# Performance work log

Hardware: AMD Instinct MI355X
Metric: run time of the kernel (lower is better)

The kernel has to match this reference:

```python
import jax, jax.numpy as jnp
import numpy as np

B, S, D, E, K = 4, 4096, 2048, 64, 2


def setup_inputs() -> dict:
    key = jax.random.key(0)
    kx, kwg, kwn, kn = jax.random.split(key, 4)
    scale = 1.0 / np.sqrt(D)
    return {
        "x": jax.random.normal(kx, (B, S, D), dtype=jnp.float32),
        "Wg": jax.random.normal(kwg, (E, D), dtype=jnp.float32) * scale,
        "bg": jnp.zeros((E,), dtype=jnp.float32),
        "Wn": jax.random.normal(kwn, (E, D), dtype=jnp.float32) * scale,
        "bn": jnp.zeros((E,), dtype=jnp.float32),
        "noise": jax.random.normal(kn, (B, S, E), dtype=jnp.float32),
    }


def reference(x, Wg, bg, Wn, bn, noise):
    # gate / noise projections: [B,S,D] @ [D,E] -> [B,S,E]
    gate_logits = jnp.einsum("bsd,ed->bse", x, Wg) + bg
    noise_std = jax.nn.softplus(jnp.einsum("bsd,ed->bse", x, Wn) + bn)
    noisy_logits = gate_logits + noise * noise_std  # training-mode path

    # top-k over experts, then scatter back with -inf elsewhere
    flat = noisy_logits.reshape(-1, E)  # [T, E], T = B*S
    top_vals, top_idx = jax.lax.top_k(flat, K)  # [T, K]
    T = flat.shape[0]
    neg_inf = jnp.full((T, E), -jnp.inf, dtype=flat.dtype)
    full_logits = neg_inf.at[jnp.arange(T)[:, None], top_idx].set(top_vals)

    gate_probs = jax.nn.softmax(full_logits, axis=-1).reshape(B, S, E)
    top_k_indices = top_idx.reshape(B, S, K)
    return gate_probs, top_k_indices
```

## Files before the change

### kernel.cpp

```cpp
#include <hip/hip_runtime.h>
#include <math.h>
#include <stdint.h>

#define D_ 2048
#define E_ 64
#define T_ 16384

#define BM 64
#define BK 64
#define NT 32
#define ABUF_B 16384
#define BBUF_B 32768
#define BUF_B (ABUF_B + BBUF_B)
#define CT_STRIDE 132

typedef _Float16 h8 __attribute__((ext_vector_type(8)));
typedef float f16v __attribute__((ext_vector_type(16)));

__device__ __forceinline__ void split2(const float4& a, const float4& b,
                                       h8& h, h8& m) {
    const float xe[8] = {a.x, a.y, a.z, a.w, b.x, b.y, b.z, b.w};
#pragma unroll
    for (int i = 0; i < 8; ++i) {
        const _Float16 hh_ = (_Float16)xe[i];
        const float r = (xe[i] - (float)hh_) * 1024.0f;
        h[i] = hh_;
        m[i] = (_Float16)r;
    }
}

__device__ __forceinline__ void gload16(const void* g, void* l) {
    __builtin_amdgcn_global_load_lds(
        (const __attribute__((address_space(1))) uint32_t*)g,
        (__attribute__((address_space(3))) uint32_t*)l, 16, 0, 0);
}

__device__ __forceinline__ void topk_epilogue(float g, float nl, float nz,
                                              int lane, size_t tg,
                                              float* __restrict__ out_probs,
                                              float* __restrict__ out_idx) {
    const float sp = fmaxf(nl, 0.f) + log1pf(expf(-fabsf(nl)));
    const float noisy = g + nz * sp;

    float v = noisy;
    int idx = lane;
#pragma unroll
    for (int off = 32; off > 0; off >>= 1) {
        const float ov = __shfl_xor(v, off);
        const int oi = __shfl_xor(idx, off);
        if (ov > v || (ov == v && oi < idx)) { v = ov; idx = oi; }
    }
    const float v1 = v;
    const int i1 = idx;
    v = (lane == i1) ? -INFINITY : noisy;
    idx = lane;
#pragma unroll
    for (int off = 32; off > 0; off >>= 1) {
        const float ov = __shfl_xor(v, off);
        const int oi = __shfl_xor(idx, off);
        if (ov > v || (ov == v && oi < idx)) { v = ov; idx = oi; }
    }
    const float v2 = v;
    const int i2 = idx;

    const float e2 = expf(v2 - v1);
    const float denom = 1.f + e2;
    const float p = (lane == i1) ? (1.f / denom)
                                 : ((lane == i2) ? (e2 / denom) : 0.f);
    out_probs[tg * E_ + lane] = p;
    if (lane == 0) {
        out_idx[tg * 2 + 0] = (float)i1;
        out_idx[tg * 2 + 1] = (float)i2;
    }
}

__global__ void w_split_kernel(const float* __restrict__ Wg,
                               const float* __restrict__ Wn,
                               h8* __restrict__ wsp) {
    const int idx = blockIdx.x * blockDim.x + threadIdx.x;
    const int lane = idx & 63;
    const int s = (idx >> 6) & 127;
    const int f = idx >> 13;
    const int n = f * 32 + (lane & 31);
    const int k0 = s * 16 + ((lane >> 5) << 3);
    const float* src = (n < 64) ? &Wg[(size_t)n * D_ + k0]
                                : &Wn[(size_t)(n - 64) * D_ + k0];
    h8 hv, mv;
#pragma unroll
    for (int i = 0; i < 8; ++i) {
        const float w = src[i];
        const _Float16 wh = (_Float16)w;
        const float r = (w - (float)wh) * 1024.0f;
        hv[i] = wh;
        mv[i] = (_Float16)r;
    }
    wsp[0 * 32768 + idx] = hv;
    wsp[1 * 32768 + idx] = mv;
}

__launch_bounds__(512)
__global__ void gemm_topk_kernel(const float* __restrict__ x,
                                 const h8* __restrict__ wsp,
                                 const float* __restrict__ bg,
                                 const float* __restrict__ bn,
                                 const float* __restrict__ noise,
                                 float* __restrict__ out_probs,
                                 float* __restrict__ out_idx) {
    __shared__ __align__(16) char smem[2 * BUF_B];
    const int tid = threadIdx.x;
    const int lane = tid & 63;
    const int wv = tid >> 6;
    const int mh = wv >> 2;
    const int wn = wv & 3;
    const int block_m0 = blockIdx.x * BM;
    const char* wb = (const char*)wsp;

    const int smf = tid >> 8;
    const int sks = (tid >> 6) & 3;
    const int sl = tid & 63;
    const int srow = smf * 32 + (sl & 31);
    const float* asrc = x + (size_t)(block_m0 + srow) * D_
                          + sks * 16 + ((sl >> 5) << 3);
    const int aw_hi = (0 * 8 + smf * 4 + sks) * 1024 + sl * 16;
    const int aw_mid = (1 * 8 + smf * 4 + sks) * 1024 + sl * 16;

    f16v hh = {}, cx = {};

    auto STAGE_B = [&](int t, int b) {
        char* Bb = smem + b * BUF_B + ABUF_B;
#pragma unroll
        for (int j = 0; j < 4; ++j) {
            const int rid = wv * 4 + j;
            const int p = rid >> 4, f = (rid & 15) >> 2, ks = rid & 3;
            gload16(wb + ((size_t)(p * 32768 + f * 8192 + (t * 4 + ks) * 64 + lane)) * 16,
                    Bb + rid * 1024 + lane * 16);
        }
    };
    auto ALOAD = [&](int t, float4& ra, float4& rb) {
        ra = *(const float4*)(asrc + t * BK);
        rb = *(const float4*)(asrc + t * BK + 4);
    };
    auto ASPLIT = [&](const float4& ra, const float4& rb, int b) {
        h8 hv, mv;
        split2(ra, rb, hv, mv);
        char* Ab = smem + b * BUF_B;
        *(h8*)(Ab + aw_hi) = hv;
        *(h8*)(Ab + aw_mid) = mv;
    };
    auto COMPUTE = [&](int b) {
        const char* Ab = smem + b * BUF_B;
        const char* Bb = Ab + ABUF_B;
#pragma unroll
        for (int ks = 0; ks < 4; ++ks) {
            const h8 ah = *(const h8*)(Ab + (0 * 8 + mh * 4 + ks) * 1024 + lane * 16);
            const h8 am = *(const h8*)(Ab + (1 * 8 + mh * 4 + ks) * 1024 + lane * 16);
            const h8 bh = *(const h8*)(Bb + (0 * 16 + wn * 4 + ks) * 1024 + lane * 16);
            const h8 bm = *(const h8*)(Bb + (1 * 16 + wn * 4 + ks) * 1024 + lane * 16);
            hh = __builtin_amdgcn_mfma_f32_32x32x16_f16(ah, bh, hh, 0, 0, 0);
            cx = __builtin_amdgcn_mfma_f32_32x32x16_f16(ah, bm, cx, 0, 0, 0);
            cx = __builtin_amdgcn_mfma_f32_32x32x16_f16(am, bh, cx, 0, 0, 0);
        }
    };

    float4 ra0, rb0, ra1, rb1;
    ALOAD(0, ra0, rb0);
    STAGE_B(0, 0);
    ASPLIT(ra0, rb0, 0);
    ALOAD(1, ra0, rb0);
    __syncthreads();

#pragma unroll 1
    for (int i = 0; i < NT / 2; ++i) {
        const int t = 2 * i;
        STAGE_B(t + 1, 1);
        if (t + 2 < NT) ALOAD(t + 2, ra1, rb1);
        COMPUTE(0);
        ASPLIT(ra0, rb0, 1);
        __syncthreads();
        if (t + 2 < NT) STAGE_B(t + 2, 0);
        if (t + 3 < NT) ALOAD(t + 3, ra0, rb0);
        COMPUTE(1);
        if (t + 2 < NT) ASPLIT(ra1, rb1, 0);
        __syncthreads();
    }

    float* Ct = (float*)smem;
    {
        const float S1 = 1.0f / 1024.0f;
        const int col = wn * 32 + (lane & 31);
        const int rbase = 4 * (lane >> 5);
#pragma unroll
        for (int r = 0; r < 16; ++r) {
            const int row = mh * 32 + (r & 3) + 8 * (r >> 2) + rbase;
            Ct[row * CT_STRIDE + col] = hh[r] + cx[r] * S1;
        }
    }
    __syncthreads();

    const float my_bg = bg[lane];
    const float my_bn = bn[lane];
#pragma unroll 1
    for (int tt = 0; tt < 8; ++tt) {
        const int tl = wv * 8 + tt;
        const size_t tg = (size_t)block_m0 + tl;
        const float g = Ct[tl * CT_STRIDE + lane] + my_bg;
        const float nl = Ct[tl * CT_STRIDE + 64 + lane] + my_bn;
        const float nz = noise[tg * E_ + lane];
        topk_epilogue(g, nl, nz, lane, tg, out_probs, out_idx);
    }
}

#define FBM 64
#define FBK 32
#define XS_STRIDE 68
#define WS_STRIDE 132
#define FCT_STRIDE 132

__launch_bounds__(256)
__global__ void noisy_topk_f32_kernel(const float* __restrict__ x,
                                      const float* __restrict__ Wg,
                                      const float* __restrict__ bg,
                                      const float* __restrict__ Wn,
                                      const float* __restrict__ bn,
                                      const float* __restrict__ noise,
                                      float* __restrict__ out_probs,
                                      float* __restrict__ out_idx) {
    __shared__ float smem[FBM * FCT_STRIDE];
    float* Xs = smem;
    float* Ws = smem + FBK * XS_STRIDE;

    const int tid = threadIdx.x;
    const int block_m0 = blockIdx.x * FBM;
    const int n0 = (tid & 31) * 4;
    const int m0 = (tid >> 5) * 8;

    float acc[8][4];
#pragma unroll
    for (int i = 0; i < 8; ++i)
#pragma unroll
        for (int j = 0; j < 4; ++j) acc[i][j] = 0.f;

    const int sj = tid & 7;
    const int sr = tid >> 3;

    for (int k0 = 0; k0 < D_; k0 += FBK) {
        __syncthreads();
#pragma unroll
        for (int it = 0; it < 2; ++it) {
            const int m = sr + it * 32;
            const float4 v = *reinterpret_cast<const float4*>(
                &x[(size_t)(block_m0 + m) * D_ + k0 + 4 * sj]);
            Xs[(4 * sj + 0) * XS_STRIDE + m] = v.x;
            Xs[(4 * sj + 1) * XS_STRIDE + m] = v.y;
            Xs[(4 * sj + 2) * XS_STRIDE + m] = v.z;
            Xs[(4 * sj + 3) * XS_STRIDE + m] = v.w;
        }
#pragma unroll
        for (int it = 0; it < 4; ++it) {
            const int n = sr + it * 32;
            const float* wrow = (n < 64) ? &Wg[(size_t)n * D_] : &Wn[(size_t)(n - 64) * D_];
            const float4 v = *reinterpret_cast<const float4*>(&wrow[k0 + 4 * sj]);
            Ws[(4 * sj + 0) * WS_STRIDE + n] = v.x;
            Ws[(4 * sj + 1) * WS_STRIDE + n] = v.y;
            Ws[(4 * sj + 2) * WS_STRIDE + n] = v.z;
            Ws[(4 * sj + 3) * WS_STRIDE + n] = v.w;
        }
        __syncthreads();
#pragma unroll
        for (int k = 0; k < FBK; ++k) {
            const float4 a0 = *reinterpret_cast<const float4*>(&Xs[k * XS_STRIDE + m0]);
            const float4 a1 = *reinterpret_cast<const float4*>(&Xs[k * XS_STRIDE + m0 + 4]);
            const float4 b4 = *reinterpret_cast<const float4*>(&Ws[k * WS_STRIDE + n0]);
            const float am[8] = {a0.x, a0.y, a0.z, a0.w, a1.x, a1.y, a1.z, a1.w};
            const float bb[4] = {b4.x, b4.y, b4.z, b4.w};
#pragma unroll
            for (int i = 0; i < 8; ++i)
#pragma unroll
                for (int j = 0; j < 4; ++j)
                    acc[i][j] = fmaf(am[i], bb[j], acc[i][j]);
        }
    }

    __syncthreads();
    float* Ct = smem;
#pragma unroll
    for (int i = 0; i < 8; ++i)
#pragma unroll
        for (int j = 0; j < 4; ++j)
            Ct[(m0 + i) * FCT_STRIDE + n0 + j] = acc[i][j];
    __syncthreads();

    const int wave = tid >> 6;
    const int lane = tid & 63;
    const float my_bg = bg[lane];
    const float my_bn = bn[lane];
#pragma unroll 1
    for (int tt = 0; tt < 16; ++tt) {
        const int tl = wave * 16 + tt;
        const size_t tg = (size_t)block_m0 + tl;
        const float g = Ct[tl * FCT_STRIDE + lane] + my_bg;
        const float nl = Ct[tl * FCT_STRIDE + 64 + lane] + my_bn;
        const float nz = noise[tg * E_ + lane];
        topk_epilogue(g, nl, nz, lane, tg, out_probs, out_idx);
    }
}

extern "C" void kernel_launch(void* const* d_in, const int* in_sizes, int n_in,
                              void* d_out, int out_size, void* d_ws, size_t ws_size,
                              hipStream_t stream) {
    const float* x = (const float*)d_in[0];
    const float* Wg = (const float*)d_in[1];
    const float* bg = (const float*)d_in[2];
    const float* Wn = (const float*)d_in[3];
    const float* bn = (const float*)d_in[4];
    const float* noise = (const float*)d_in[5];
    float* out_probs = (float*)d_out;
    float* out_idx = out_probs + (size_t)T_ * E_;

    const size_t WSP_BYTES = (size_t)2 * 32768 * 16;
    if (ws_size >= WSP_BYTES) {
        h8* wsp = (h8*)d_ws;
        hipLaunchKernelGGL(w_split_kernel, dim3(128), dim3(256), 0, stream, Wg, Wn, wsp);
        hipLaunchKernelGGL(gemm_topk_kernel, dim3(T_ / BM), dim3(512), 0, stream,
                           x, wsp, bg, bn, noise, out_probs, out_idx);
    } else {
        hipLaunchKernelGGL(noisy_topk_f32_kernel, dim3(T_ / FBM), dim3(256), 0, stream,
                           x, Wg, bg, Wn, bn, noise, out_probs, out_idx);
    }
}
```

Measured before the change: 59.00 us.

## Triple-buffer LDS staging with fine-grained vmcnt waits in GEMM loop

Moves the shared-memory pipeline from two stages to three. The weight tile is now staged two steps ahead, and the x loads run further ahead too. The full __syncthreads calls become explicit s_waitcnt vmcnt counts plus s_barrier, so global loads stay in flight across the barriers and load latency hides behind MFMA compute. The cost is 50% more LDS (144KB), which may limit occupancy to one block per CU. The hand-picked vmcnt counts must also match the number of outstanding loads, or the pipeline will be wrong.

Result: no change. 58.52 us (-0.8%).

```diff
diff --git a/kernel.cpp b/kernel.cpp
--- a/kernel.cpp
+++ b/kernel.cpp
@@ -12,6 +12,7 @@
 #define ABUF_B 16384
 #define BBUF_B 32768
 #define BUF_B (ABUF_B + BBUF_B)
+#define NBUF 3
 #define CT_STRIDE 132
 
 typedef _Float16 h8 __attribute__((ext_vector_type(8)));
@@ -106,7 +107,7 @@
                                  const float* __restrict__ noise,
                                  float* __restrict__ out_probs,
                                  float* __restrict__ out_idx) {
-    __shared__ __align__(16) char smem[2 * BUF_B];
+    __shared__ __align__(16) char smem[NBUF * BUF_B];
     const int tid = threadIdx.x;
     const int lane = tid & 63;
     const int wv = tid >> 6;
@@ -166,24 +167,40 @@
     ALOAD(0, ra0, rb0);
     STAGE_B(0, 0);
     ASPLIT(ra0, rb0, 0);
+    STAGE_B(1, 1);
     ALOAD(1, ra0, rb0);
-    __syncthreads();
+    ALOAD(2, ra1, rb1);
+    asm volatile("s_waitcnt vmcnt(8) lgkmcnt(0)" ::: "memory");
+    __builtin_amdgcn_s_barrier();
+    __builtin_amdgcn_sched_barrier(0);
 
 #pragma unroll 1
     for (int i = 0; i < NT / 2; ++i) {
         const int t = 2 * i;
-        STAGE_B(t + 1, 1);
-        if (t + 2 < NT) ALOAD(t + 2, ra1, rb1);
-        COMPUTE(0);
-        ASPLIT(ra0, rb0, 1);
-        __syncthreads();
-        if (t + 2 < NT) STAGE_B(t + 2, 0);
-        if (t + 3 < NT) ALOAD(t + 3, ra0, rb0);
-        COMPUTE(1);
-        if (t + 2 < NT) ASPLIT(ra1, rb1, 0);
-        __syncthreads();
-    }
-
+        {
+            if (t + 2 < NT) STAGE_B(t + 2, (t + 2) % NBUF);
+            COMPUTE(t % NBUF);
+            ASPLIT(ra0, rb0, (t + 1) % NBUF);
+            if (t + 3 < NT) ALOAD(t + 3, ra0, rb0);
+            if (t < NT - 2) asm volatile("s_waitcnt vmcnt(6) lgkmcnt(0)" ::: "memory");
+            else            asm volatile("s_waitcnt vmcnt(0) lgkmcnt(0)" ::: "memory");
+            __builtin_amdgcn_s_barrier();
+            __builtin_amdgcn_sched_barrier(0);
+        }
+        {
+            const int u = t + 1;
+            if (u + 2 < NT) STAGE_B(u + 2, (u + 2) % NBUF);
+            COMPUTE(u % NBUF);
+            if (u + 1 < NT) ASPLIT(ra1, rb1, (u + 1) % NBUF);
+            if (u + 3 < NT) ALOAD(u + 3, ra1, rb1);
+            if (u < NT - 2) asm volatile("s_waitcnt vmcnt(6) lgkmcnt(0)" ::: "memory");
+            else            asm volatile("s_waitcnt vmcnt(0) lgkmcnt(0)" ::: "memory");
+            __builtin_amdgcn_s_barrier();
+            __builtin_amdgcn_sched_barrier(0);
+        }
+    }
+
+    __syncthreads();
     float* Ct = (float*)smem;
     {
         const float S1 = 1.0f / 1024.0f;
```
